# Optimization experiments

Measured on AMD Instinct MI355X. Metric: run time of the kernel, lower is better.

The kernel has to match this reference:

```python
import jax, jax.numpy as jnp
import numpy as np

N = 50000
S = 32           # n_sample
D_IN = 256
D_OUT = 128
ALPHA = 0.2      # leakyrelu negative slope


def setup_inputs() -> dict:
    key = jax.random.key(0)
    k1, k2, k3, k4 = jax.random.split(key, 4)
    x = jax.random.normal(k1, (N, D_IN), dtype=jnp.float32)
    neibs = jax.random.randint(k2, (N, S), 0, N, dtype=jnp.int64)
    # xavier_uniform with gain=1.414
    limW = 1.414 * np.sqrt(6.0 / (D_IN + D_OUT))
    W = jax.random.uniform(k3, (D_IN, D_OUT), dtype=jnp.float32, minval=-limW, maxval=limW)
    lima = 1.414 * np.sqrt(6.0 / (2 * D_OUT + 1))
    a = jax.random.uniform(k4, (2 * D_OUT, 1), dtype=jnp.float32, minval=-lima, maxval=lima)
    return {"x": x, "neibs": neibs, "W": W, "a": a}


def reference(x, neibs, W, a):
    # x: [N, D_in], neibs: [N, S] int, W: [D_in, D_out], a: [2*D_out, 1]
    xw = x @ W                                  # [N, D_out]
    xn = xw[neibs]                              # [N, S, D_out] gathered neighbor feats
    # a_input @ a == xw @ a[:D_out] + xn @ a[D_out:]  (avoid materializing concat)
    a_self = a[:D_OUT, 0]                       # [D_out]
    a_neib = a[D_OUT:, 0]                       # [D_out]
    e = (xw @ a_self)[:, None] + jnp.einsum('nsd,d->ns', xn, a_neib)  # [N, S]
    e = jnp.where(e > 0, e, ALPHA * e)          # leakyrelu
    attention = jax.nn.softmax(e, axis=1)       # [N, S]  (dropout skipped: eval mode)
    h_prime = jnp.einsum('ns,nsd->nd', attention, xn)                # [N, D_out]
    output = jnp.concatenate([xw, h_prime], axis=1)                  # concat=True
    return jax.nn.elu(output)
```

## Files before the change

### kernel.cpp

```cpp
#include <hip/hip_runtime.h>
#include <math.h>

#define N_NODES 50000
#define S_NEIB 32
#define D_IN 256
#define D_OUT 128
#define ALPHA 0.2f

typedef __attribute__((ext_vector_type(8))) short bf16x8;
typedef __attribute__((ext_vector_type(4))) float f32x4;

__device__ __forceinline__ float elu_f(float v) {
    return v > 0.f ? v : (expf(v) - 1.f);
}

__device__ __forceinline__ unsigned short f2bf(float f) {
    unsigned u = __builtin_bit_cast(unsigned, f);
    u += 0x7fffu + ((u >> 16) & 1u);
    return (unsigned short)(u >> 16);
}

__global__ __launch_bounds__(256) void pack_w_kernel(
    const float* __restrict__ W, unsigned short* __restrict__ Wp)
{
    int tid = blockIdx.x * 256 + threadIdx.x;
    int j  = tid & 7;
    int t  = (tid >> 3) & 15;
    int kb = (tid >> 7) & 31;
    int c  = tid >> 12;
    Wp[tid] = f2bf(W[(kb * 8 + j) * D_OUT + c * 16 + t]);
}

__global__ __launch_bounds__(256) void gemm_score_kernel(
    const float* __restrict__ x, const unsigned short* __restrict__ Wp,
    const float* __restrict__ a, unsigned short* __restrict__ xwb,
    float* __restrict__ s_self, float* __restrict__ s_neib,
    float* __restrict__ out)
{
    __shared__ unsigned short xs[64 * 264];
    __shared__ float ps[2][4][64];

    const int tid  = threadIdx.x;
    const int lane = tid & 63;
    const int wave = tid >> 6;
    const int q    = lane >> 4;
    const int t    = lane & 15;
    const int colW = wave * 32;
    const int r0   = blockIdx.x * 64;

    for (int i = 0; i < 16; ++i) {
        int f4  = i * 256 + tid;
        int row = f4 >> 6;
        int c4  = (f4 & 63) << 2;
        float4 v = make_float4(0.f, 0.f, 0.f, 0.f);
        if (r0 + row < N_NODES)
            v = *(const float4*)(x + (size_t)(r0 + row) * D_IN + c4);
        ushort4 b;
        b.x = f2bf(v.x); b.y = f2bf(v.y); b.z = f2bf(v.z); b.w = f2bf(v.w);
        *(ushort4*)&xs[row * 264 + c4] = b;
    }
    __syncthreads();

    const bf16x8* Wp8 = (const bf16x8*)Wp;

    f32x4 acc[4][2];
    #pragma unroll
    for (int mt = 0; mt < 4; ++mt)
        #pragma unroll
        for (int nt = 0; nt < 2; ++nt)
            acc[mt][nt] = (f32x4){0.f, 0.f, 0.f, 0.f};

    #pragma unroll
    for (int kc = 0; kc < 8; ++kc) {
        const int k0 = kc * 32 + q * 8;
        bf16x8 afrag[4];
        #pragma unroll
        for (int mt = 0; mt < 4; ++mt)
            afrag[mt] = *(const bf16x8*)&xs[(mt * 16 + t) * 264 + k0];
        bf16x8 bfrag[2];
        #pragma unroll
        for (int nt = 0; nt < 2; ++nt)
            bfrag[nt] = Wp8[((wave * 2 + nt) * 32 + kc * 4 + q) * 16 + t];
        #pragma unroll
        for (int mt = 0; mt < 4; ++mt)
            #pragma unroll
            for (int nt = 0; nt < 2; ++nt)
                acc[mt][nt] = __builtin_amdgcn_mfma_f32_16x16x32_bf16(
                    afrag[mt], bfrag[nt], acc[mt][nt], 0, 0, 0);
    }

    const float as0 = a[colW + t],         as1 = a[colW + 16 + t];
    const float an0 = a[D_OUT + colW + t], an1 = a[D_OUT + colW + 16 + t];
    #pragma unroll
    for (int mt = 0; mt < 4; ++mt) {
        #pragma unroll
        for (int r = 0; r < 4; ++r) {
            float vs = acc[mt][0][r] * as0 + acc[mt][1][r] * as1;
            float vn = acc[mt][0][r] * an0 + acc[mt][1][r] * an1;
            #pragma unroll
            for (int d = 8; d >= 1; d >>= 1) {
                vs += __shfl_xor(vs, d);
                vn += __shfl_xor(vn, d);
            }
            if (t == 0) {
                int row = mt * 16 + q * 4 + r;
                ps[0][wave][row] = vs;
                ps[1][wave][row] = vn;
            }
        }
    }
    __syncthreads();
    if (tid < 64 && r0 + tid < N_NODES) {
        s_self[r0 + tid] = ps[0][0][tid] + ps[0][1][tid] + ps[0][2][tid] + ps[0][3][tid];
        s_neib[r0 + tid] = ps[1][0][tid] + ps[1][1][tid] + ps[1][2][tid] + ps[1][3][tid];
    }

    #pragma unroll
    for (int mt = 0; mt < 4; ++mt) {
        #pragma unroll
        for (int r = 0; r < 4; ++r) {
            int g = r0 + mt * 16 + q * 4 + r;
            if (g < N_NODES) {
                #pragma unroll
                for (int nt = 0; nt < 2; ++nt) {
                    int col = colW + nt * 16 + t;
                    float v = acc[mt][nt][r];
                    xwb[(size_t)g * D_OUT + col] = f2bf(v);
                    out[(size_t)g * (2 * D_OUT) + col] = elu_f(v);
                }
            }
        }
    }
}

__global__ __launch_bounds__(256, 4) void aggregate_kernel(
    const int* __restrict__ neibs, const unsigned short* __restrict__ xwb,
    const float* __restrict__ s_self, const float* __restrict__ s_neib,
    float* __restrict__ out)
{
    const int lane = threadIdx.x & 63;
    const int wave = threadIdx.x >> 6;
    const int n = blockIdx.x * 4 + wave;
    if (n >= N_NODES) return;

    const int half = lane >> 5;
    const int hl   = lane & 31;

    int   idx = 0;
    float e   = -1e30f;
    if (lane < 32) {
        idx = neibs[n * S_NEIB + lane];
        e = s_self[n] + s_neib[idx];
        e = e > 0.f ? e : ALPHA * e;
    }
    float m = e;
    #pragma unroll
    for (int d = 16; d >= 1; d >>= 1) m = fmaxf(m, __shfl_xor(m, d));
    float p = (lane < 32) ? __expf(e - m) : 0.f;
    float ssum = p;
    #pragma unroll
    for (int d = 16; d >= 1; d >>= 1) ssum += __shfl_xor(ssum, d);
    float att = p / ssum;

    float a0 = 0.f, a1 = 0.f, a2 = 0.f, a3 = 0.f;
    #pragma unroll
    for (int s2 = 0; s2 < 16; ++s2) {
        int   s = s2 * 2 + half;
        int   j = __shfl(idx, s);
        float w = __shfl(att, s);
        uint2 v = *(const uint2*)(xwb + (size_t)j * D_OUT + 4 * hl);
        float f0 = __builtin_bit_cast(float, v.x << 16);
        float f1 = __builtin_bit_cast(float, v.x & 0xffff0000u);
        float f2 = __builtin_bit_cast(float, v.y << 16);
        float f3 = __builtin_bit_cast(float, v.y & 0xffff0000u);
        a0 = fmaf(w, f0, a0);
        a1 = fmaf(w, f1, a1);
        a2 = fmaf(w, f2, a2);
        a3 = fmaf(w, f3, a3);
    }
    a0 += __shfl_xor(a0, 32);
    a1 += __shfl_xor(a1, 32);
    a2 += __shfl_xor(a2, 32);
    a3 += __shfl_xor(a3, 32);

    if (half == 0) {
        float4 o;
        o.x = elu_f(a0);
        o.y = elu_f(a1);
        o.z = elu_f(a2);
        o.w = elu_f(a3);
        *(float4*)(out + (size_t)n * (2 * D_OUT) + D_OUT + 4 * hl) = o;
    }
}

extern "C" void kernel_launch(void* const* d_in, const int* in_sizes, int n_in,
                              void* d_out, int out_size, void* d_ws, size_t ws_size,
                              hipStream_t stream) {
    const float* x     = (const float*)d_in[0];
    const int*   neibs = (const int*)  d_in[1];
    const float* W     = (const float*)d_in[2];
    const float* a     = (const float*)d_in[3];
    float* out = (float*)d_out;

    unsigned short* xwb = (unsigned short*)d_ws;
    float* s_self = (float*)(xwb + (size_t)N_NODES * D_OUT);
    float* s_neib = s_self + N_NODES;
    unsigned short* Wp = (unsigned short*)(s_neib + N_NODES);

    pack_w_kernel<<<128, 256, 0, stream>>>(W, Wp);
    gemm_score_kernel<<<(N_NODES + 63) / 64, 256, 0, stream>>>(
        x, Wp, a, xwb, s_self, s_neib, out);
    aggregate_kernel<<<(N_NODES + 3) / 4, 256, 0, stream>>>(
        neibs, xwb, s_self, s_neib, out);
}
```

Measured before the change: 163.9 us.

## Process two nodes per wave in aggregation with software-pipelined neighbor gathers

The aggregate kernel now maps each half-wave to its own node, so one wave handles two nodes. This removes the idle upper half-lanes in the softmax and the cross-half reduction at the end. The neighbor-row gathers are issued in batches of eight with the next batch prefetched into registers, so more loads are in flight at once. The cost is higher register pressure from the cur/nxt buffers under launch bounds (256,4), and N must be even.

```diff
diff --git a/kernel.cpp b/kernel.cpp
--- a/kernel.cpp
+++ b/kernel.cpp
@@ -18,6 +18,13 @@
     unsigned u = __builtin_bit_cast(unsigned, f);
     u += 0x7fffu + ((u >> 16) & 1u);
     return (unsigned short)(u >> 16);
+}
+
+__device__ __forceinline__ float bflo(unsigned v) {
+    return __builtin_bit_cast(float, v << 16);
+}
+__device__ __forceinline__ float bfhi(unsigned v) {
+    return __builtin_bit_cast(float, v & 0xffff0000u);
 }
 
 __global__ __launch_bounds__(256) void pack_w_kernel(
@@ -138,59 +145,67 @@
     const float* __restrict__ s_self, const float* __restrict__ s_neib,
     float* __restrict__ out)
 {
-    const int lane = threadIdx.x & 63;
-    const int wave = threadIdx.x >> 6;
-    const int n = blockIdx.x * 4 + wave;
-    if (n >= N_NODES) return;
+    const int lane  = threadIdx.x & 63;
+    const int wavei = threadIdx.x >> 6;
+    const int n0 = (blockIdx.x * 4 + wavei) * 2;
+    if (n0 >= N_NODES) return;
 
     const int half = lane >> 5;
     const int hl   = lane & 31;
-
-    int   idx = 0;
-    float e   = -1e30f;
-    if (lane < 32) {
-        idx = neibs[n * S_NEIB + lane];
-        e = s_self[n] + s_neib[idx];
-        e = e > 0.f ? e : ALPHA * e;
-    }
+    const int node = n0 + half;
+    const int srcb = lane & 32;
+
+    int   idx = neibs[n0 * S_NEIB + lane];
+    float e   = s_self[node] + s_neib[idx];
+    e = e > 0.f ? e : ALPHA * e;
+
     float m = e;
     #pragma unroll
     for (int d = 16; d >= 1; d >>= 1) m = fmaxf(m, __shfl_xor(m, d));
-    float p = (lane < 32) ? __expf(e - m) : 0.f;
+    float p = __expf(e - m);
     float ssum = p;
     #pragma unroll
     for (int d = 16; d >= 1; d >>= 1) ssum += __shfl_xor(ssum, d);
     float att = p / ssum;
 
+    const unsigned short* colp = xwb + 4 * hl;
+
     float a0 = 0.f, a1 = 0.f, a2 = 0.f, a3 = 0.f;
-    #pragma unroll
-    for (int s2 = 0; s2 < 16; ++s2) {
-        int   s = s2 * 2 + half;
-        int   j = __shfl(idx, s);
-        float w = __shfl(att, s);
-        uint2 v = *(const uint2*)(xwb + (size_t)j * D_OUT + 4 * hl);
-        float f0 = __builtin_bit_cast(float, v.x << 16);
-        float f1 = __builtin_bit_cast(float, v.x & 0xffff0000u);
-        float f2 = __builtin_bit_cast(float, v.y << 16);
-        float f3 = __builtin_bit_cast(float, v.y & 0xffff0000u);
-        a0 = fmaf(w, f0, a0);
-        a1 = fmaf(w, f1, a1);
-        a2 = fmaf(w, f2, a2);
-        a3 = fmaf(w, f3, a3);
-    }
-    a0 += __shfl_xor(a0, 32);
-    a1 += __shfl_xor(a1, 32);
-    a2 += __shfl_xor(a2, 32);
-    a3 += __shfl_xor(a3, 32);
-
-    if (half == 0) {
-        float4 o;
-        o.x = elu_f(a0);
-        o.y = elu_f(a1);
-        o.z = elu_f(a2);
-        o.w = elu_f(a3);
-        *(float4*)(out + (size_t)n * (2 * D_OUT) + D_OUT + 4 * hl) = o;
-    }
+    uint2 cur[8], nxt[8];
+
+    #pragma unroll
+    for (int i = 0; i < 8; ++i) {
+        int j = __shfl(idx, srcb + i);
+        cur[i] = *(const uint2*)(colp + (size_t)j * D_OUT);
+    }
+    #pragma unroll
+    for (int b = 0; b < 4; ++b) {
+        if (b < 3) {
+            #pragma unroll
+            for (int i = 0; i < 8; ++i) {
+                int j = __shfl(idx, srcb + (b + 1) * 8 + i);
+                nxt[i] = *(const uint2*)(colp + (size_t)j * D_OUT);
+            }
+        }
+        #pragma unroll
+        for (int i = 0; i < 8; ++i) {
+            float w = __shfl(att, srcb + b * 8 + i);
+            uint2 v = cur[i];
+            a0 = fmaf(w, bflo(v.x), a0);
+            a1 = fmaf(w, bfhi(v.x), a1);
+            a2 = fmaf(w, bflo(v.y), a2);
+            a3 = fmaf(w, bfhi(v.y), a3);
+        }
+        #pragma unroll
+        for (int i = 0; i < 8; ++i) cur[i] = nxt[i];
+    }
+
+    float4 o;
+    o.x = elu_f(a0);
+    o.y = elu_f(a1);
+    o.z = elu_f(a2);
+    o.w = elu_f(a3);
+    *(float4*)(out + (size_t)node * (2 * D_OUT) + D_OUT + 4 * hl) = o;
 }
 
 extern "C" void kernel_launch(void* const* d_in, const int* in_sizes, int n_in,
@@ -210,6 +225,6 @@
     pack_w_kernel<<<128, 256, 0, stream>>>(W, Wp);
     gemm_score_kernel<<<(N_NODES + 63) / 64, 256, 0, stream>>>(
         x, Wp, a, xwb, s_self, s_neib, out);
-    aggregate_kernel<<<(N_NODES + 3) / 4, 256, 0, stream>>>(
+    aggregate_kernel<<<(N_NODES + 7) / 8, 256, 0, stream>>>(
         neibs, xwb, s_self, s_neib, out);
 }
```

Measured after the change: 163.4 us. Within noise of the previous version (-0.3%).
